# Kernel tuning notes

Measured on AMD Instinct MI355X. Metric: run time of the kernel, lower is better.

## Reference

```python
import jax, jax.numpy as jnp
import numpy as np

NUM_HEADS = 12


def setup_inputs() -> dict:
    key = jax.random.key(0)
    k1, k2, k3 = jax.random.split(key, 3)
    B, S, E = 1, 4096, 768
    x = jax.random.normal(k1, (B, S, E), dtype=jnp.float32)
    # learned parameters (nn.Linear weights, stored as [in, out] for x @ W)
    w_qkv = jax.random.normal(k2, (E, 3 * E), dtype=jnp.float32) * 0.02
    b_qkv = jnp.zeros((3 * E,), dtype=jnp.float32)
    w_out = jax.random.normal(k3, (E, E), dtype=jnp.float32) * 0.02
    b_out = jnp.zeros((E,), dtype=jnp.float32)
    return {"x": x, "w_qkv": w_qkv, "b_qkv": b_qkv, "w_out": w_out, "b_out": b_out}


def reference(x, w_qkv, b_qkv, w_out, b_out):
    """Single-process (world_size==1) path of the module:
    qkv projection -> multi-head scaled-dot-product softmax attention
    (non-causal) -> output projection. Dropout is identity in eval.
    """
    B, S, E = x.shape
    H = NUM_HEADS
    D = E // H
    scale = 1.0 / jnp.sqrt(jnp.asarray(D, dtype=x.dtype))

    qkv = x @ w_qkv + b_qkv                       # [B, S, 3E]
    qkv = qkv.reshape(B, S, 3, H, D)
    qkv = jnp.transpose(qkv, (2, 0, 3, 1, 4))     # [3, B, H, S, D]
    q, k, v = qkv[0], qkv[1], qkv[2]

    scores = jnp.einsum("bhqd,bhkd->bhqk", q * scale, k)  # [B, H, S, S]
    attn = jax.nn.softmax(scores, axis=-1)
    out = jnp.einsum("bhqk,bhkd->bhqd", attn, v)           # [B, H, S, D]

    out = jnp.transpose(out, (0, 2, 1, 3)).reshape(B, S, E)
    return out @ w_out + b_out
```

## Files before the change

### kernel.cpp

```cpp
#include <hip/hip_runtime.h>

typedef __attribute__((ext_vector_type(8))) short bh8;
typedef __attribute__((ext_vector_type(4))) float fx4;

__device__ __forceinline__ unsigned short f2bf(float f) {
    unsigned int u = __float_as_uint(f);
    u += 0x7FFF + ((u >> 16) & 1);
    return (unsigned short)(u >> 16);
}

__device__ __forceinline__ unsigned int cvtpk_bf16(float a, float b) {
    unsigned int r;
    asm("v_cvt_pk_bf16_f32 %0, %1, %2" : "=v"(r) : "v"(a), "v"(b));
    return r;
}

__device__ __forceinline__ bh8 pack4(unsigned int a, unsigned int b,
                                     unsigned int c, unsigned int d) {
    union { unsigned int u[4]; bh8 h; } z;
    z.u[0] = a; z.u[1] = b; z.u[2] = c; z.u[3] = d;
    return z.h;
}

__device__ __forceinline__ void stage_rows8(const unsigned short* g, long ldg,
                                            unsigned short* lds, int lane) {
    int r8 = lane >> 3;
    int gc = (lane & 7) ^ r8;
    __builtin_amdgcn_global_load_lds(
        (const __attribute__((address_space(1))) void*)(g + (long)r8 * ldg + gc * 8),
        (__attribute__((address_space(3))) void*)lds, 16, 0, 0);
}

__device__ __forceinline__ bh8 frag_ld(const unsigned short* t, int row, int kchunk, int lane) {
    int ch = (kchunk + (lane >> 4)) ^ (row & 7);
    return *(const bh8*)(t + row * 64 + ch * 8);
}

__global__ __launch_bounds__(256) void castbf(const float* __restrict__ x,
                                              unsigned short* __restrict__ y, int n) {
    int i = (blockIdx.x * 256 + threadIdx.x) * 4;
    if (i < n) {
        float4 v = *(const float4*)(x + i);
        ushort4 o = make_ushort4(f2bf(v.x), f2bf(v.y), f2bf(v.z), f2bf(v.w));
        *(ushort4*)(y + i) = o;
    }
}

__global__ __launch_bounds__(256) void transW(const float* __restrict__ W,
                                              unsigned short* __restrict__ Wt,
                                              int K, int N) {
    __shared__ float t[32][33];
    const int n0 = blockIdx.x * 32, k0 = blockIdx.y * 32;
    const int tx = threadIdx.x & 31, ty = threadIdx.x >> 5;
    #pragma unroll
    for (int r = ty; r < 32; r += 8)
        t[r][tx] = W[(size_t)(k0 + r) * N + n0 + tx];
    __syncthreads();
    #pragma unroll
    for (int r = ty; r < 32; r += 8)
        Wt[(size_t)(n0 + r) * K + k0 + tx] = f2bf(t[tx][r]);
}

__global__ __launch_bounds__(256) void transV(const unsigned short* __restrict__ qkv,
                                              unsigned short* __restrict__ vt) {
    __shared__ unsigned short t[64][65];
    const int s0 = blockIdx.x * 64, h = blockIdx.y;
    const int tx = threadIdx.x & 63, ty = threadIdx.x >> 6;
    #pragma unroll
    for (int r = ty; r < 64; r += 4)
        t[r][tx] = qkv[(size_t)(s0 + r) * 2304 + 1536 + h * 64 + tx];
    __syncthreads();
    const int px = (tx & 32) + ((tx & 16) >> 2) + ((tx & 12) << 1) + (tx & 3);
    #pragma unroll
    for (int r = ty; r < 64; r += 4)
        vt[((size_t)h * 64 + r) * 4096 + s0 + px] = t[tx][r];
}

template <int OUT_BF16, int SCALE_Q>
__global__ __launch_bounds__(256) void gemm128(const unsigned short* __restrict__ A,
                                               const unsigned short* __restrict__ Bt,
                                               const float* __restrict__ bias,
                                               void* __restrict__ Cout,
                                               int M, int N, int K) {
    __shared__ __align__(16) unsigned short Ash[128 * 64];
    __shared__ __align__(16) unsigned short Bsh[128 * 64];
    const int m0 = blockIdx.y * 128, n0 = blockIdx.x * 128;
    const int tid = threadIdx.x, wid = tid >> 6, lane = tid & 63;
    const int wr = (wid >> 1) * 64, wc = (wid & 1) * 64;

    fx4 acc[4][4];
    #pragma unroll
    for (int i = 0; i < 4; ++i)
        #pragma unroll
        for (int j = 0; j < 4; ++j)
            acc[i][j] = (fx4){0.f, 0.f, 0.f, 0.f};

    for (int k0 = 0; k0 < K; k0 += 64) {
        #pragma unroll
        for (int g = 0; g < 4; ++g) {
            int rt = (wid * 4 + g) * 8;
            stage_rows8(A + (size_t)(m0 + rt) * K + k0, K, Ash + rt * 64, lane);
            stage_rows8(Bt + (size_t)(n0 + rt) * K + k0, K, Bsh + rt * 64, lane);
        }
        __syncthreads();
        #pragma unroll
        for (int ks = 0; ks < 2; ++ks) {
            bh8 af[4], bfr[4];
            #pragma unroll
            for (int i = 0; i < 4; ++i) af[i] = frag_ld(Ash, wr + i * 16 + (lane & 15), ks * 4, lane);
            #pragma unroll
            for (int j = 0; j < 4; ++j) bfr[j] = frag_ld(Bsh, wc + j * 16 + (lane & 15), ks * 4, lane);
            #pragma unroll
            for (int i = 0; i < 4; ++i)
                #pragma unroll
                for (int j = 0; j < 4; ++j)
                    acc[i][j] = __builtin_amdgcn_mfma_f32_16x16x32_bf16(af[i], bfr[j], acc[i][j], 0, 0, 0);
        }
        __syncthreads();
    }

    const int cc = lane & 15, g4 = (lane >> 4) * 4;
    #pragma unroll
    for (int j = 0; j < 4; ++j) {
        int col = n0 + wc + j * 16 + cc;
        float bv = bias[col];
        float sc = (SCALE_Q && col < 768) ? 0.18033688011112042f : 1.0f;
        #pragma unroll
        for (int i = 0; i < 4; ++i) {
            #pragma unroll
            for (int r = 0; r < 4; ++r) {
                int row = m0 + wr + i * 16 + g4 + r;
                float v = (acc[i][j][r] + bv) * sc;
                if (OUT_BF16)
                    ((unsigned short*)Cout)[(size_t)row * N + col] = f2bf(v);
                else
                    ((float*)Cout)[(size_t)row * N + col] = v;
            }
        }
    }
}

__global__ __launch_bounds__(256) void gemm64(const unsigned short* __restrict__ A,
                                              const unsigned short* __restrict__ Bt,
                                              const float* __restrict__ bias,
                                              float* __restrict__ Cout,
                                              int M, int N, int K) {
    __shared__ __align__(16) unsigned short Ash[64 * 64];
    __shared__ __align__(16) unsigned short Bsh[64 * 64];
    const int m0 = blockIdx.y * 64, n0 = blockIdx.x * 64;
    const int tid = threadIdx.x, wid = tid >> 6, lane = tid & 63;
    const int wr = (wid >> 1) * 32, wc = (wid & 1) * 32;

    fx4 acc[2][2];
    #pragma unroll
    for (int i = 0; i < 2; ++i)
        #pragma unroll
        for (int j = 0; j < 2; ++j)
            acc[i][j] = (fx4){0.f, 0.f, 0.f, 0.f};

    for (int k0 = 0; k0 < K; k0 += 64) {
        #pragma unroll
        for (int g = 0; g < 2; ++g) {
            int rt = (wid * 2 + g) * 8;
            stage_rows8(A + (size_t)(m0 + rt) * K + k0, K, Ash + rt * 64, lane);
            stage_rows8(Bt + (size_t)(n0 + rt) * K + k0, K, Bsh + rt * 64, lane);
        }
        __syncthreads();
        #pragma unroll
        for (int ks = 0; ks < 2; ++ks) {
            bh8 af[2], bfr[2];
            #pragma unroll
            for (int i = 0; i < 2; ++i) af[i] = frag_ld(Ash, wr + i * 16 + (lane & 15), ks * 4, lane);
            #pragma unroll
            for (int j = 0; j < 2; ++j) bfr[j] = frag_ld(Bsh, wc + j * 16 + (lane & 15), ks * 4, lane);
            #pragma unroll
            for (int i = 0; i < 2; ++i)
                #pragma unroll
                for (int j = 0; j < 2; ++j)
                    acc[i][j] = __builtin_amdgcn_mfma_f32_16x16x32_bf16(af[i], bfr[j], acc[i][j], 0, 0, 0);
        }
        __syncthreads();
    }

    const int cc = lane & 15, g4 = (lane >> 4) * 4;
    #pragma unroll
    for (int j = 0; j < 2; ++j) {
        int col = n0 + wc + j * 16 + cc;
        float bv = bias[col];
        #pragma unroll
        for (int i = 0; i < 2; ++i) {
            #pragma unroll
            for (int r = 0; r < 4; ++r) {
                int row = m0 + wr + i * 16 + g4 + r;
                Cout[(size_t)row * N + col] = acc[i][j][r] + bv;
            }
        }
    }
}

__global__ __launch_bounds__(256) void attn_fwd(const unsigned short* __restrict__ qkv,
                                                const unsigned short* __restrict__ vt,
                                                unsigned short* __restrict__ ao) {
    __shared__ __align__(16) unsigned short Qs[64 * 64];
    __shared__ __align__(16) unsigned short Ks[2][64 * 64];
    __shared__ __align__(16) unsigned short Vs[2][64 * 64];
    const int h = blockIdx.y, q0 = blockIdx.x * 64;
    const int tid = threadIdx.x, wid = tid >> 6, lane = tid & 63;
    const int g = lane >> 4, qc = lane & 15, x = qc & 7;

    const unsigned short* qg  = qkv + (size_t)q0 * 2304 + h * 64;
    const unsigned short* kgb = qkv + 768 + h * 64;
    const unsigned short* vgb = vt + (size_t)h * 64 * 4096;

    #pragma unroll
    for (int gg = 0; gg < 2; ++gg) {
        int rt = (wid * 2 + gg) * 8;
        stage_rows8(qg  + (size_t)rt * 2304, 2304, Qs + rt * 64, lane);
        stage_rows8(kgb + (size_t)rt * 2304, 2304, &Ks[0][rt * 64], lane);
        stage_rows8(vgb + (size_t)rt * 4096, 4096, &Vs[0][rt * 64], lane);
    }
    __syncthreads();

    const int qrow = wid * 16 + qc;
    const bh8 qf0 = frag_ld(Qs, qrow, 0, lane);
    const bh8 qf1 = frag_ld(Qs, qrow, 4, lane);

    int koff[4][2], voff[4][2];
    #pragma unroll
    for (int jm = 0; jm < 4; ++jm)
        #pragma unroll
        for (int kc = 0; kc < 2; ++kc)
            koff[jm][kc] = (16 * jm + qc) * 64 + ((4 * kc + g) ^ x) * 8;
    #pragma unroll
    for (int dj = 0; dj < 4; ++dj)
        #pragma unroll
        for (int ks = 0; ks < 2; ++ks)
            voff[dj][ks] = (16 * dj + qc) * 64 + ((4 * ks + g) ^ x) * 8;

    float l_run = 0.f;
    fx4 oac[4];
    #pragma unroll
    for (int dj = 0; dj < 4; ++dj) oac[dj] = (fx4){0.f, 0.f, 0.f, 0.f};

    const unsigned short* knext = kgb + (size_t)64 * 2304;
    const unsigned short* vnext = vgb + 64;

    auto tile_step = [&](const unsigned short* Kc, const unsigned short* Vc,
                         unsigned short* Kd, unsigned short* Vd, bool pref) {
        if (pref) {
            #pragma unroll
            for (int gg = 0; gg < 2; ++gg) {
                int rt = (wid * 2 + gg) * 8;
                stage_rows8(knext + (size_t)rt * 2304, 2304, Kd + rt * 64, lane);
                stage_rows8(vnext + (size_t)rt * 4096, 4096, Vd + rt * 64, lane);
            }
            knext += (size_t)64 * 2304;
            vnext += 64;
        }

        fx4 sT[4];
        __builtin_amdgcn_s_setprio(1);
        #pragma unroll
        for (int jm = 0; jm < 4; ++jm) {
            bh8 kf0 = *(const bh8*)(Kc + koff[jm][0]);
            bh8 kf1 = *(const bh8*)(Kc + koff[jm][1]);
            fx4 z = (fx4){0.f, 0.f, 0.f, 0.f};
            z = __builtin_amdgcn_mfma_f32_16x16x32_bf16(kf0, qf0, z, 0, 0, 0);
            z = __builtin_amdgcn_mfma_f32_16x16x32_bf16(kf1, qf1, z, 0, 0, 0);
            sT[jm] = z;
        }
        __builtin_amdgcn_s_setprio(0);

        #pragma unroll
        for (int jm = 0; jm < 4; ++jm) {
            sT[jm][0] = __builtin_amdgcn_exp2f(sT[jm][0]);
            sT[jm][1] = __builtin_amdgcn_exp2f(sT[jm][1]);
            sT[jm][2] = __builtin_amdgcn_exp2f(sT[jm][2]);
            sT[jm][3] = __builtin_amdgcn_exp2f(sT[jm][3]);
            l_run += (sT[jm][0] + sT[jm][1]) + (sT[jm][2] + sT[jm][3]);
        }

        __builtin_amdgcn_s_setprio(1);
        #pragma unroll
        for (int ks = 0; ks < 2; ++ks) {
            bh8 pb = pack4(cvtpk_bf16(sT[2 * ks][0],     sT[2 * ks][1]),
                           cvtpk_bf16(sT[2 * ks][2],     sT[2 * ks][3]),
                           cvtpk_bf16(sT[2 * ks + 1][0], sT[2 * ks + 1][1]),
                           cvtpk_bf16(sT[2 * ks + 1][2], sT[2 * ks + 1][3]));
            #pragma unroll
            for (int dj = 0; dj < 4; ++dj) {
                bh8 vf = *(const bh8*)(Vc + voff[dj][ks]);
                oac[dj] = __builtin_amdgcn_mfma_f32_16x16x32_bf16(vf, pb, oac[dj], 0, 0, 0);
            }
        }
        __builtin_amdgcn_s_setprio(0);
        __syncthreads();
    };

    for (int t2 = 0; t2 < 32; ++t2) {
        tile_step(Ks[0], Vs[0], Ks[1], Vs[1], true);
        tile_step(Ks[1], Vs[1], Ks[0], Vs[0], t2 < 31);
    }

    l_run += __shfl_xor(l_run, 16);
    l_run += __shfl_xor(l_run, 32);
    const float inv = 1.0f / l_run;
    unsigned short* aop = ao + (size_t)(q0 + qrow) * 768 + h * 64;
    #pragma unroll
    for (int dj = 0; dj < 4; ++dj) {
        int d0 = dj * 16 + 4 * g;
        *(unsigned int*)(aop + d0)     = cvtpk_bf16(oac[dj][0] * inv, oac[dj][1] * inv);
        *(unsigned int*)(aop + d0 + 2) = cvtpk_bf16(oac[dj][2] * inv, oac[dj][3] * inv);
    }
}

extern "C" void kernel_launch(void* const* d_in, const int* in_sizes, int n_in,
                              void* d_out, int out_size, void* d_ws, size_t ws_size,
                              hipStream_t stream) {
    const float* x     = (const float*)d_in[0];
    const float* w_qkv = (const float*)d_in[1];
    const float* b_qkv = (const float*)d_in[2];
    const float* w_out = (const float*)d_in[3];
    const float* b_out = (const float*)d_in[4];
    float* out = (float*)d_out;

    const int S = 4096, E = 768, E3 = 2304, H = 12;

    unsigned short* xb    = (unsigned short*)d_ws;
    unsigned short* wqkvT = xb    + (size_t)S * E;
    unsigned short* woutT = wqkvT + (size_t)E3 * E;
    unsigned short* qkvb  = woutT + (size_t)E * E;
    unsigned short* vtp   = qkvb  + (size_t)S * E3;
    unsigned short* ao    = vtp   + (size_t)H * 64 * S;

    castbf<<<dim3((S * E) / (256 * 4)), 256, 0, stream>>>(x, xb, S * E);
    transW<<<dim3(E3 / 32, E / 32), 256, 0, stream>>>(w_qkv, wqkvT, E, E3);
    transW<<<dim3(E / 32, E / 32), 256, 0, stream>>>(w_out, woutT, E, E);
    gemm128<1, 1><<<dim3(E3 / 128, S / 128), 256, 0, stream>>>(xb, wqkvT, b_qkv, qkvb, S, E3, E);
    transV<<<dim3(S / 64, H), 256, 0, stream>>>(qkvb, vtp);
    attn_fwd<<<dim3(S / 64, H), 256, 0, stream>>>(qkvb, vtp, ao);
    gemm64<<<dim3(E / 64, S / 64), 256, 0, stream>>>(ao, woutT, b_out, out, S, E, E);
}
```

Measured before the change: 137.5 us.

## Split attention work 2x2 across waves over query and key halves with LDS reduction

Attention waves are rearranged so each wave handles 32 query rows and half of each 64-key tile, instead of 16 query rows over the full tile. Each K and V fragment loaded from LDS is now reused across two query groups, which halves per-wave LDS fragment traffic. Partial outputs and row sums are combined at the end through an LDS reduction that reuses the staging buffer. The cost is more accumulator registers per wave plus an extra barrier and reduction step at the end.

```diff
diff --git a/kernel.cpp b/kernel.cpp
--- a/kernel.cpp
+++ b/kernel.cpp
@@ -201,46 +201,57 @@
 __global__ __launch_bounds__(256) void attn_fwd(const unsigned short* __restrict__ qkv,
                                                 const unsigned short* __restrict__ vt,
                                                 unsigned short* __restrict__ ao) {
-    __shared__ __align__(16) unsigned short Qs[64 * 64];
-    __shared__ __align__(16) unsigned short Ks[2][64 * 64];
-    __shared__ __align__(16) unsigned short Vs[2][64 * 64];
+    __shared__ __align__(16) char smem[40960];
+    unsigned short* Qs  = (unsigned short*)smem;
+    unsigned short* Ks0 = (unsigned short*)(smem + 8192);
+    unsigned short* Ks1 = (unsigned short*)(smem + 16384);
+    unsigned short* Vs0 = (unsigned short*)(smem + 24576);
+    unsigned short* Vs1 = (unsigned short*)(smem + 32768);
+    float* Of    = (float*)smem;
+    float* l_lds = (float*)(smem + 17408);
+
     const int h = blockIdx.y, q0 = blockIdx.x * 64;
     const int tid = threadIdx.x, wid = tid >> 6, lane = tid & 63;
     const int g = lane >> 4, qc = lane & 15, x = qc & 7;
-
-    const unsigned short* qg  = qkv + (size_t)q0 * 2304 + h * 64;
+    const int wq = wid >> 1, wk = wid & 1;
+
+    const unsigned short* qg_  = qkv + (size_t)q0 * 2304 + h * 64;
     const unsigned short* kgb = qkv + 768 + h * 64;
     const unsigned short* vgb = vt + (size_t)h * 64 * 4096;
 
     #pragma unroll
     for (int gg = 0; gg < 2; ++gg) {
         int rt = (wid * 2 + gg) * 8;
-        stage_rows8(qg  + (size_t)rt * 2304, 2304, Qs + rt * 64, lane);
-        stage_rows8(kgb + (size_t)rt * 2304, 2304, &Ks[0][rt * 64], lane);
-        stage_rows8(vgb + (size_t)rt * 4096, 4096, &Vs[0][rt * 64], lane);
+        stage_rows8(qg_ + (size_t)rt * 2304, 2304, Qs + rt * 64, lane);
+        stage_rows8(kgb + (size_t)rt * 2304, 2304, Ks0 + rt * 64, lane);
+        stage_rows8(vgb + (size_t)rt * 4096, 4096, Vs0 + rt * 64, lane);
     }
     __syncthreads();
 
-    const int qrow = wid * 16 + qc;
-    const bh8 qf0 = frag_ld(Qs, qrow, 0, lane);
-    const bh8 qf1 = frag_ld(Qs, qrow, 4, lane);
-
-    int koff[4][2], voff[4][2];
-    #pragma unroll
-    for (int jm = 0; jm < 4; ++jm)
+    bh8 qf[2][2];
+    #pragma unroll
+    for (int qg = 0; qg < 2; ++qg)
         #pragma unroll
         for (int kc = 0; kc < 2; ++kc)
-            koff[jm][kc] = (16 * jm + qc) * 64 + ((4 * kc + g) ^ x) * 8;
+            qf[qg][kc] = frag_ld(Qs, 32 * wq + 16 * qg + qc, 4 * kc, lane);
+
+    int koff[2][2], voff[4];
+    #pragma unroll
+    for (int jm = 0; jm < 2; ++jm)
+        #pragma unroll
+        for (int kc = 0; kc < 2; ++kc)
+            koff[jm][kc] = (32 * wk + 16 * jm + qc) * 64 + ((4 * kc + g) ^ x) * 8;
     #pragma unroll
     for (int dj = 0; dj < 4; ++dj)
-        #pragma unroll
-        for (int ks = 0; ks < 2; ++ks)
-            voff[dj][ks] = (16 * dj + qc) * 64 + ((4 * ks + g) ^ x) * 8;
-
-    float l_run = 0.f;
-    fx4 oac[4];
-    #pragma unroll
-    for (int dj = 0; dj < 4; ++dj) oac[dj] = (fx4){0.f, 0.f, 0.f, 0.f};
+        voff[dj] = (16 * dj + qc) * 64 + ((4 * wk + g) ^ x) * 8;
+
+    float lrun[2] = {0.f, 0.f};
+    fx4 oacP[4][2];
+    #pragma unroll
+    for (int dj = 0; dj < 4; ++dj)
+        #pragma unroll
+        for (int qg = 0; qg < 2; ++qg)
+            oacP[dj][qg] = (fx4){0.f, 0.f, 0.f, 0.f};
 
     const unsigned short* knext = kgb + (size_t)64 * 2304;
     const unsigned short* vnext = vgb + 64;
@@ -258,59 +269,90 @@
             vnext += 64;
         }
 
-        fx4 sT[4];
+        bh8 kf[2][2];
+        #pragma unroll
+        for (int jm = 0; jm < 2; ++jm) {
+            kf[jm][0] = *(const bh8*)(Kc + koff[jm][0]);
+            kf[jm][1] = *(const bh8*)(Kc + koff[jm][1]);
+        }
+        fx4 sT[2][2];
         __builtin_amdgcn_s_setprio(1);
         #pragma unroll
-        for (int jm = 0; jm < 4; ++jm) {
-            bh8 kf0 = *(const bh8*)(Kc + koff[jm][0]);
-            bh8 kf1 = *(const bh8*)(Kc + koff[jm][1]);
-            fx4 z = (fx4){0.f, 0.f, 0.f, 0.f};
-            z = __builtin_amdgcn_mfma_f32_16x16x32_bf16(kf0, qf0, z, 0, 0, 0);
-            z = __builtin_amdgcn_mfma_f32_16x16x32_bf16(kf1, qf1, z, 0, 0, 0);
-            sT[jm] = z;
-        }
+        for (int jm = 0; jm < 2; ++jm)
+            #pragma unroll
+            for (int qg = 0; qg < 2; ++qg) {
+                fx4 z = (fx4){0.f, 0.f, 0.f, 0.f};
+                z = __builtin_amdgcn_mfma_f32_16x16x32_bf16(kf[jm][0], qf[qg][0], z, 0, 0, 0);
+                z = __builtin_amdgcn_mfma_f32_16x16x32_bf16(kf[jm][1], qf[qg][1], z, 0, 0, 0);
+                sT[jm][qg] = z;
+            }
         __builtin_amdgcn_s_setprio(0);
 
         #pragma unroll
-        for (int jm = 0; jm < 4; ++jm) {
-            sT[jm][0] = __builtin_amdgcn_exp2f(sT[jm][0]);
-            sT[jm][1] = __builtin_amdgcn_exp2f(sT[jm][1]);
-            sT[jm][2] = __builtin_amdgcn_exp2f(sT[jm][2]);
-            sT[jm][3] = __builtin_amdgcn_exp2f(sT[jm][3]);
-            l_run += (sT[jm][0] + sT[jm][1]) + (sT[jm][2] + sT[jm][3]);
-        }
-
+        for (int jm = 0; jm < 2; ++jm)
+            #pragma unroll
+            for (int qg = 0; qg < 2; ++qg) {
+                sT[jm][qg][0] = __builtin_amdgcn_exp2f(sT[jm][qg][0]);
+                sT[jm][qg][1] = __builtin_amdgcn_exp2f(sT[jm][qg][1]);
+                sT[jm][qg][2] = __builtin_amdgcn_exp2f(sT[jm][qg][2]);
+                sT[jm][qg][3] = __builtin_amdgcn_exp2f(sT[jm][qg][3]);
+                lrun[qg] += (sT[jm][qg][0] + sT[jm][qg][1]) + (sT[jm][qg][2] + sT[jm][qg][3]);
+            }
+
+        bh8 vf[4];
+        #pragma unroll
+        for (int dj = 0; dj < 4; ++dj) vf[dj] = *(const bh8*)(Vc + voff[dj]);
         __builtin_amdgcn_s_setprio(1);
         #pragma unroll
-        for (int ks = 0; ks < 2; ++ks) {
-            bh8 pb = pack4(cvtpk_bf16(sT[2 * ks][0],     sT[2 * ks][1]),
-                           cvtpk_bf16(sT[2 * ks][2],     sT[2 * ks][3]),
-                           cvtpk_bf16(sT[2 * ks + 1][0], sT[2 * ks + 1][1]),
-                           cvtpk_bf16(sT[2 * ks + 1][2], sT[2 * ks + 1][3]));
+        for (int qg = 0; qg < 2; ++qg) {
+            bh8 pb = pack4(cvtpk_bf16(sT[0][qg][0], sT[0][qg][1]),
+                           cvtpk_bf16(sT[0][qg][2], sT[0][qg][3]),
+                           cvtpk_bf16(sT[1][qg][0], sT[1][qg][1]),
+                           cvtpk_bf16(sT[1][qg][2], sT[1][qg][3]));
+            #pragma unroll
+            for (int dj = 0; dj < 4; ++dj)
+                oacP[dj][qg] = __builtin_amdgcn_mfma_f32_16x16x32_bf16(vf[dj], pb, oacP[dj][qg], 0, 0, 0);
+        }
+        __builtin_amdgcn_s_setprio(0);
+        __syncthreads();
+    };
+
+    for (int t2 = 0; t2 < 32; ++t2) {
+        tile_step(Ks0, Vs0, Ks1, Vs1, true);
+        tile_step(Ks1, Vs1, Ks0, Vs0, t2 < 31);
+    }
+
+    #pragma unroll
+    for (int qg = 0; qg < 2; ++qg) {
+        lrun[qg] += __shfl_xor(lrun[qg], 16);
+        lrun[qg] += __shfl_xor(lrun[qg], 32);
+    }
+    if (wk == 1) {
+        #pragma unroll
+        for (int qg = 0; qg < 2; ++qg) {
+            int q = 32 * wq + 16 * qg + qc;
+            #pragma unroll
+            for (int dj = 0; dj < 4; ++dj)
+                *(fx4*)(Of + q * 68 + 16 * dj + 4 * g) = oacP[dj][qg];
+            l_lds[q] = lrun[qg];
+        }
+    }
+    __syncthreads();
+    if (wk == 0) {
+        #pragma unroll
+        for (int qg = 0; qg < 2; ++qg) {
+            int q = 32 * wq + 16 * qg + qc;
+            float inv = 1.0f / (lrun[qg] + l_lds[q]);
+            unsigned short* aop = ao + (size_t)(q0 + q) * 768 + h * 64;
             #pragma unroll
             for (int dj = 0; dj < 4; ++dj) {
-                bh8 vf = *(const bh8*)(Vc + voff[dj][ks]);
-                oac[dj] = __builtin_amdgcn_mfma_f32_16x16x32_bf16(vf, pb, oac[dj], 0, 0, 0);
-            }
-        }
-        __builtin_amdgcn_s_setprio(0);
-        __syncthreads();
-    };
-
-    for (int t2 = 0; t2 < 32; ++t2) {
-        tile_step(Ks[0], Vs[0], Ks[1], Vs[1], true);
-        tile_step(Ks[1], Vs[1], Ks[0], Vs[0], t2 < 31);
-    }
-
-    l_run += __shfl_xor(l_run, 16);
-    l_run += __shfl_xor(l_run, 32);
-    const float inv = 1.0f / l_run;
-    unsigned short* aop = ao + (size_t)(q0 + qrow) * 768 + h * 64;
-    #pragma unroll
-    for (int dj = 0; dj < 4; ++dj) {
-        int d0 = dj * 16 + 4 * g;
-        *(unsigned int*)(aop + d0)     = cvtpk_bf16(oac[dj][0] * inv, oac[dj][1] * inv);
-        *(unsigned int*)(aop + d0 + 2) = cvtpk_bf16(oac[dj][2] * inv, oac[dj][3] * inv);
+                fx4 o = oacP[dj][qg];
+                fx4 p = *(const fx4*)(Of + q * 68 + 16 * dj + 4 * g);
+                int d0 = dj * 16 + 4 * g;
+                *(unsigned int*)(aop + d0)     = cvtpk_bf16((o[0] + p[0]) * inv, (o[1] + p[1]) * inv);
+                *(unsigned int*)(aop + d0 + 2) = cvtpk_bf16((o[2] + p[2]) * inv, (o[3] + p[3]) * inv);
+            }
+        }
     }
 }
 
```

After: 131.0 us. -4.7%, faster.
